# Performance work log

Hardware: AMD Instinct MI355X
Metric: run time of the kernel (lower is better)

Reference implementation:

```python
import jax, jax.numpy as jnp
import numpy as np

# Dims matching init_kwargs / input_specs
H = 64   # latent_size (GRU hidden)
L = 64   # rnn_layers
D = 128  # input_size
B = 128  # batch
T = 256  # sequence length


def setup_inputs() -> dict:
    key = jax.random.key(0)
    ks = jax.random.split(key, 13)
    s = 1.0 / np.sqrt(H)  # PyTorch GRU/Linear default init scale
    u = lambda k, shp: jax.random.uniform(k, shp, jnp.float32, -s, s)
    return {
        "context": jax.random.normal(ks[0], (B, T, D), jnp.float32),
        # encoder GRU params; layer 0 consumes D, layers 1..L-1 consume H
        "enc_Wih0": u(ks[1], (3 * H, D)),
        "enc_Wih": u(ks[2], (L - 1, 3 * H, H)),
        "enc_Whh": u(ks[3], (L, 3 * H, H)),
        "enc_bih": u(ks[4], (L, 3 * H)),
        "enc_bhh": u(ks[5], (L, 3 * H)),
        # decoder GRU params
        "dec_Wih0": u(ks[6], (3 * H, D)),
        "dec_Wih": u(ks[7], (L - 1, 3 * H, H)),
        "dec_Whh": u(ks[8], (L, 3 * H, H)),
        "dec_bih": u(ks[9], (L, 3 * H)),
        "dec_bhh": u(ks[10], (L, 3 * H)),
        # output projection
        "Wo": u(ks[11], (D, H)),
        "bo": u(ks[12], (D,)),
    }


def _gru_cell(x, h, Wih, Whh, bih, bhh):
    # PyTorch gate order: r, z, n
    gi = x @ Wih.T + bih            # (B, 3H)
    gh = h @ Whh.T + bhh            # (B, 3H)
    ir, iz, inn = jnp.split(gi, 3, axis=-1)
    hr, hz, hn = jnp.split(gh, 3, axis=-1)
    r = jax.nn.sigmoid(ir + hr)
    z = jax.nn.sigmoid(iz + hz)
    n = jnp.tanh(inn + r * hn)
    return (1.0 - z) * n + z * h


def _run_gru(X, h0, Wih0, Wih, Whh, bih, bhh):
    # X: (B, T, D); h0: (L, B, H). Returns (top-layer outputs (B,T,H), final hidden (L,B,H)).
    def layer_step(x_in, lp):
        h_prev, W_ih, W_hh, b_i, b_h = lp
        h_new = _gru_cell(x_in, h_prev, W_ih, W_hh, b_i, b_h)
        return h_new, h_new

    @jax.checkpoint
    def step(hs, x_t):
        h_first = _gru_cell(x_t, hs[0], Wih0, Whh[0], bih[0], bhh[0])
        top, hs_rest = jax.lax.scan(
            layer_step, h_first, (hs[1:], Wih, Whh[1:], bih[1:], bhh[1:]))
        return jnp.concatenate([h_first[None], hs_rest], axis=0), top

    hs_final, outs = jax.lax.scan(step, h0, jnp.swapaxes(X, 0, 1))
    return jnp.swapaxes(outs, 0, 1), hs_final


def reference(context, enc_Wih0, enc_Wih, enc_Whh, enc_bih, enc_bhh,
              dec_Wih0, dec_Wih, dec_Whh, dec_bih, dec_bhh, Wo, bo):
    Bc = context.shape[0]
    h0 = jnp.zeros((L, Bc, H), context.dtype)
    # encoder: only final hidden state is used
    _, h_n = _run_gru(context, h0, enc_Wih0, enc_Wih, enc_Whh, enc_bih, enc_bhh)
    # teacher forcing (ratio=1.0): decoder input at step i is X[:, i-1], zeros at i=0
    dec_in = jnp.concatenate([jnp.zeros_like(context[:, :1]), context[:, :-1]], axis=1)
    dec_out, _ = _run_gru(dec_in, h_n, dec_Wih0, dec_Wih, dec_Whh, dec_bih, dec_bhh)
    return dec_out @ Wo.T + bo  # (B, T, D)
```

## Files before the change

kernel.cpp:

```cpp
#include <hip/hip_runtime.h>
#include <stdint.h>

typedef uint16_t u16;
typedef unsigned long long u64;
typedef __attribute__((ext_vector_type(8))) short short8;
typedef __attribute__((ext_vector_type(4))) float f32x4;

#define SCOPE __HIP_MEMORY_SCOPE_AGENT
#define FSTRIDE 16
#define FLD(p) __hip_atomic_load((p), __ATOMIC_RELAXED, SCOPE)
#define FST(p, v) __hip_atomic_store((p), (v), __ATOMIC_RELAXED, SCOPE)

template <int N> struct IC { static constexpr int value = N; };

static __device__ __forceinline__ float bf2f(u16 b) {
  union { uint32_t u; float f; } x; x.u = ((uint32_t)b) << 16; return x.f;
}
static __device__ __forceinline__ u16 f2bf(float f) {
  union { float f; uint32_t u; } x; x.f = f;
  uint32_t u = x.u;
  u += 0x7fffu + ((u >> 16) & 1u);
  return (u16)(u >> 16);
}
static __device__ __forceinline__ float sigm(float x) {
  return __builtin_amdgcn_rcpf(1.f + __expf(-x));
}
static __device__ __forceinline__ float tanhf_(float x) {
  return 1.f - 2.f * __builtin_amdgcn_rcpf(1.f + __expf(2.f * x));
}
static __device__ __forceinline__ void lds_barrier() {
  asm volatile("s_waitcnt lgkmcnt(0)\n\ts_barrier" ::: "memory");
}
#define DRAIN0() asm volatile("s_waitcnt vmcnt(0)" ::: "memory")
static __device__ __forceinline__ int imin(int a, int b) { return a < b ? a : b; }

#define OFF_WHA 0
#define OFF_WHB 12288
#define OFF_WIB 24576
#define OFF_WIA 36864
#define OFF_WO  49152

template <int CHE, int CHD>
__global__ __launch_bounds__(256, 1) void gru_pipeline(
    const void* ctx_,
    const void* eWih0_, const void* eWih_, const void* eWhh_,
    const void* ebih_,  const void* ebhh_,
    const void* dWih0_, const void* dWih_, const void* dWhh_,
    const void* dbih_,  const void* dbhh_,
    const void* Wo_,    const void* bo_,   void* out_,
    int* __restrict__ pflag, int* __restrict__ cflag,
    u64* __restrict__ xbufW, int RW, int RE)
{
  const int tid  = threadIdx.x;
  const int lane = tid & 63;
  const int q    = tid >> 6;
  const int lo   = lane & 15;
  const int hi   = lane >> 4;
  const int blk  = blockIdx.x;
  const int P    = blk >> 3;
  const int g    = blk & 7;
  const int LA   = 2 * P;
  const int LB   = 2 * P + 1;
  const int NKCA = (P == 0) ? 4 : 2;
  u64* xbufE = (u64*)out_;

  extern __shared__ __align__(16) u16 dynlds[];

  __shared__ __align__(16) u16 hbA[2][16 * 72];
  __shared__ __align__(16) u16 hbB[2][16 * 72];
  __shared__ __align__(16) u16 xstA[2][16 * 72];
  __shared__ int s_cnt, s_fin, s_cn;
  if (tid == 0) { s_cnt = 0; s_fin = 0; s_cn = 0; }
  for (int i = tid; i < 16 * 72; i += 256) {
    hbA[0][i] = 0; hbA[1][i] = 0; hbB[0][i] = 0; hbB[1][i] = 0;
    xstA[0][i] = 0; xstA[1][i] = 0;
  }
  __syncthreads();
  {
    u16 v = ((const u16*)ebih_)[2 * tid];
    int e = (v >> 7) & 0xFF;
    if (e >= 100 && e <= 126) atomicAdd(&s_cnt, 1);
  }
  __syncthreads();
  const bool bf = (s_cnt >= 128);

  auto ld8 = [&](const void* p, int idx) -> short8 {
    if (bf) return *(const short8*)((const u16*)p + idx);
    const float* f = (const float*)p + idx;
    short8 r;
#pragma unroll
    for (int j = 0; j < 8; ++j) r[j] = (short)f2bf(f[j]);
    return r;
  };
  auto ld1 = [&](const void* p, int idx) -> float {
    return bf ? bf2f(((const u16*)p)[idx]) : ((const float*)p)[idx];
  };

  const int T0 = q, T1 = 4 + q, T2 = 8 + q;

  short8 zf8 = {0,0,0,0,0,0,0,0};
  float  bov[2] = {0.f, 0.f};
  float brzA[2], binA, bhnA;
  float brzB[2], binB, bhnB;

  auto stage_w = [&](int offU16, const void* W, int gidx0, int NT, int KC, int K) {
    for (int nt = q; nt < NT; nt += 4)
      for (int kc = 0; kc < KC; ++kc) {
        short8 v = ld8(W, gidx0 + (nt*16 + lo)*K + kc*32 + hi*8);
        *(short8*)(dynlds + offU16 + (nt*KC + kc)*512 + lane*8) = v;
      }
  };

  auto load_phase = [&](int ph) {
    const void* WH  = ph ? dWhh_ : eWhh_;
    const void* WIs = ph ? dWih_ : eWih_;
    const void* WI0 = ph ? dWih0_ : eWih0_;
    const void* bi  = ph ? dbih_ : ebih_;
    const void* bh  = ph ? dbhh_ : ebhh_;
    stage_w(OFF_WHA, WH, LA*192*64, 12, 2, 64);
    stage_w(OFF_WHB, WH, LB*192*64, 12, 2, 64);
    stage_w(OFF_WIB, WIs, LA*192*64, 12, 2, 64);
    if (LA == 0) stage_w(OFF_WIA, WI0, 0, 12, 4, 128);
    else         stage_w(OFF_WIA, WIs, (LA-1)*192*64, 12, 2, 64);
    brzA[0] = ld1(bi, LA*192 + T0*16 + lo) + ld1(bh, LA*192 + T0*16 + lo);
    brzA[1] = ld1(bi, LA*192 + T1*16 + lo) + ld1(bh, LA*192 + T1*16 + lo);
    binA    = ld1(bi, LA*192 + T2*16 + lo);
    bhnA    = ld1(bh, LA*192 + T2*16 + lo);
    brzB[0] = ld1(bi, LB*192 + T0*16 + lo) + ld1(bh, LB*192 + T0*16 + lo);
    brzB[1] = ld1(bi, LB*192 + T1*16 + lo) + ld1(bh, LB*192 + T1*16 + lo);
    binB    = ld1(bi, LB*192 + T2*16 + lo);
    bhnB    = ld1(bh, LB*192 + T2*16 + lo);
  };
  load_phase(0);
  if (P == 31) {
    stage_w(OFF_WO, Wo_, 0, 8, 2, 64);
    bov[0] = ld1(bo_, 32*q + lo);
    bov[1] = ld1(bo_, 32*q + 16 + lo);
  }

  const int oWhA0 = OFF_WHA + T0*1024 + lane*8;
  const int oWhA1 = OFF_WHA + T1*1024 + lane*8;
  const int oWhA2 = OFF_WHA + T2*1024 + lane*8;
  const int oWhB0 = OFF_WHB + T0*1024 + lane*8;
  const int oWhB1 = OFF_WHB + T1*1024 + lane*8;
  const int oWhB2 = OFF_WHB + T2*1024 + lane*8;
  const int oWiB0 = OFF_WIB + T0*1024 + lane*8;
  const int oWiB1 = OFF_WIB + T1*1024 + lane*8;
  const int oWiB2 = OFF_WIB + T2*1024 + lane*8;
  const int oWiA0 = OFF_WIA + T0*(NKCA*512) + lane*8;
  const int oWiA1 = OFF_WIA + T1*(NKCA*512) + lane*8;
  const int oWiA2 = OFF_WIA + T2*(NKCA*512) + lane*8;
  const int oWo0  = OFF_WO + (2*q + 0)*1024 + lane*8;
  const int oWo1  = OFF_WO + (2*q + 1)*1024 + lane*8;

  auto WF = [&](int off, int kc) -> short8 {
    return *(const short8*)(dynlds + off + kc*512);
  };

  auto do_proj = [&](int tprev, const u16* hs) {
    f32x4 pacc[2];
#pragma unroll
    for (int ct = 0; ct < 2; ++ct) { float v = bov[ct]; f32x4 tv = {v,v,v,v}; pacc[ct] = tv; }
#pragma unroll
    for (int kc = 0; kc < 2; ++kc) {
      short8 hA = *(const short8*)(hs + lo*72 + kc*32 + hi*8);
      pacc[0] = __builtin_amdgcn_mfma_f32_16x16x32_bf16(hA, WF(oWo0, kc), pacc[0], 0, 0, 0);
      pacc[1] = __builtin_amdgcn_mfma_f32_16x16x32_bf16(hA, WF(oWo1, kc), pacc[1], 0, 0, 0);
    }
#pragma unroll
    for (int ct = 0; ct < 2; ++ct) {
      int n = 32*q + 16*ct + lo;
#pragma unroll
      for (int p = 0; p < 4; ++p) {
        int b = 16*g + hi*4 + p;
        size_t idx = ((size_t)b * 256 + (tprev - 256)) * 128 + n;
        float v = fminf(64.f, fmaxf(-64.f, pacc[ct][p]));
        if (bf) ((u16*)out_)[idx] = f2bf(v);
        else    ((float*)out_)[idx] = v;
      }
    }
  };

  float hprevA[4], hprevB[4];
#pragma unroll
  for (int p = 0; p < 4; ++p) { hprevA[p] = 0.f; hprevB[p] = 0.f; }

  const int brow = 16*g + lo;

  const int eIn  = (P > 0 ? P - 1 : 0) * 8 + g;
  const int eOut = (P < 31 ? P : 30) * 8 + g;
  int* fin   = pflag + eIn  * FSTRIDE;
  int* fout  = pflag + eOut * FSTRIDE;
  int* cself = cflag + (P * 8 + g) * FSTRIDE;
  int* cnext = cflag + ((P < 31 ? P + 1 : 31) * 8 + g) * FSTRIDE;

  int budget = 1 << 22;
  const int srow = 4 * (tid & 3);
  const int scol = tid >> 2;

  int f0 = 0, f1 = 0, f2 = 0, f3 = 0;
  int c0 = 0, c1 = 0, c2 = 0, c3 = 0;

  __syncthreads();

  auto span = [&](auto chc, const int tbase, const int cbase, const int RC, const bool dec) {
    constexpr int CH  = decltype(chc)::value;
    constexpr int PTT = (CH >= 2) ? CH - 2 : 0;
    const int NC   = 256 / CH;
    const int RM   = dec ? (RW - 1) : (RE - 1);
    const int toff = dec ? 256 : 0;
    const u64* rbi = dec ? (xbufW + (size_t)eIn  * ((size_t)RW * 256))
                         : (xbufE + (size_t)eIn  * ((size_t)RE * 256));
    u64*       rbo = dec ? (xbufW + (size_t)eOut * ((size_t)RW * 256))
                         : (xbufE + (size_t)eOut * ((size_t)RE * 256));

#pragma unroll 1
    for (int k = 0; k < NC; ++k) {
      const int ck    = cbase + k;
      const int t0    = tbase + k * CH;
      const int fneed = ck + 1;
      const int need  = (k >= RC) ? (cbase + k + 1 - RC) : 0;

      const bool slowF = (P > 0)  && (s_fin < fneed);
      const bool slowC = (P < 31) && (need > 0) && (s_cn < need);
      if (slowF || slowC) {
        if (tid == 0) {
          if (slowF) {
            int v = 0;
            while (budget > 0) {
              int a = FLD(fin + 0), b = FLD(fin + 1), c = FLD(fin + 2), d = FLD(fin + 3);
              v = imin(imin(a, b), imin(c, d));
              if (v >= fneed) break;
              --budget; __builtin_amdgcn_s_sleep(2);
            }
            s_fin = v;
          }
          if (slowC) {
            int v = 0;
            while (budget > 0) {
              int a = FLD(cnext + 0), b = FLD(cnext + 1), c = FLD(cnext + 2), d = FLD(cnext + 3);
              v = imin(imin(a, b), imin(c, d));
              if (v >= need) break;
              --budget; __builtin_amdgcn_s_sleep(2);
            }
            s_cn = v;
          }
        }
        lds_barrier();
      }

      u64 pa[CH];
#pragma unroll
      for (int j = 0; j < CH; ++j) pa[j] = 0;
      if (P > 0) {
#pragma unroll
        for (int j = 0; j < CH; ++j)
          pa[j] = FLD(rbi + (size_t)((t0 + j - toff) & RM) * 256 + tid);
      }

#pragma unroll
      for (int tt = 0; tt < CH; ++tt) {
        const int t = t0 + tt;

        if (P > 0) {
          u16* xd = xstA[t & 1];
#pragma unroll
          for (int p = 0; p < 4; ++p)
            xd[(srow + p) * 72 + scol] = (u16)(pa[tt] >> (16 * p));
        }

        lds_barrier();

        if (tt == PTT && tid == 0) {
          if (P > 0)  { f0 = FLD(fin + 0); f1 = FLD(fin + 1); f2 = FLD(fin + 2); f3 = FLD(fin + 3); }
          if (P < 31) { c0 = FLD(cnext + 0); c1 = FLD(cnext + 1); c2 = FLD(cnext + 2); c3 = FLD(cnext + 3); }
        }

        if (P == 31 && t >= 257) do_proj(t - 1, hbB[(t + 1) & 1]);

        f32x4 ar, az, ain, ahn;
        { float v;
          v = brzA[0]; ar  = (f32x4){v,v,v,v};
          v = brzA[1]; az  = (f32x4){v,v,v,v};
          v = binA;    ain = (f32x4){v,v,v,v};
          v = bhnA;    ahn = (f32x4){v,v,v,v}; }
        const u16* hsA = hbA[(t + 1) & 1];
#pragma unroll
        for (int kc = 0; kc < 2; ++kc) {
          short8 hA = *(const short8*)(hsA + lo*72 + kc*32 + hi*8);
          ar  = __builtin_amdgcn_mfma_f32_16x16x32_bf16(hA, WF(oWhA0, kc), ar,  0, 0, 0);
          az  = __builtin_amdgcn_mfma_f32_16x16x32_bf16(hA, WF(oWhA1, kc), az,  0, 0, 0);
          ahn = __builtin_amdgcn_mfma_f32_16x16x32_bf16(hA, WF(oWhA2, kc), ahn, 0, 0, 0);
        }
        short8 xfA[4] = {zf8, zf8, zf8, zf8};
        if (P > 0) {
          const u16* xs = xstA[t & 1];
#pragma unroll
          for (int kc = 0; kc < 2; ++kc)
            xfA[kc] = *(const short8*)(xs + lo*72 + kc*32 + hi*8);
        } else {
          int tx = (t < 256) ? t : ((t == 256) ? 0 : t - 257);
#pragma unroll
          for (int kc = 0; kc < 4; ++kc)
            xfA[kc] = ld8(ctx_, (brow * 256 + tx) * 128 + kc*32 + hi*8);
        }
        if (!(P == 0 && t == 256)) {
#pragma unroll
          for (int kc = 0; kc < 4; ++kc) {
            if (kc < NKCA) {
              ar  = __builtin_amdgcn_mfma_f32_16x16x32_bf16(xfA[kc], WF(oWiA0, kc), ar,  0, 0, 0);
              az  = __builtin_amdgcn_mfma_f32_16x16x32_bf16(xfA[kc], WF(oWiA1, kc), az,  0, 0, 0);
              ain = __builtin_amdgcn_mfma_f32_16x16x32_bf16(xfA[kc], WF(oWiA2, kc), ain, 0, 0, 0);
            }
          }
        }
        u16 hAb[4];
#pragma unroll
        for (int p = 0; p < 4; ++p) {
          float r = sigm(ar[p]);
          float z = sigm(az[p]);
          float n = tanhf_(ain[p] + r * ahn[p]);
          float h = n + z * (hprevA[p] - n);
          h = fminf(1.f, fmaxf(-1.f, h));
          hprevA[p] = h;
          hAb[p] = f2bf(h);
        }

        if (tt == CH - 1 && tid == 0) {
          if (P > 0)  s_fin = imin(imin(f0, f1), imin(f2, f3));
          if (P < 31) s_cn  = imin(imin(c0, c1), imin(c2, c3));
        }

        {
          u16* hd = hbA[t & 1];
#pragma unroll
          for (int p = 0; p < 4; ++p)
            hd[(hi*4 + p) * 72 + q*16 + lo] = hAb[p];
        }

        lds_barrier();

        { float v;
          v = brzB[0]; ar  = (f32x4){v,v,v,v};
          v = brzB[1]; az  = (f32x4){v,v,v,v};
          v = binB;    ain = (f32x4){v,v,v,v};
          v = bhnB;    ahn = (f32x4){v,v,v,v}; }
        const u16* hsB = hbB[(t + 1) & 1];
        const u16* xsB = hbA[t & 1];
#pragma unroll
        for (int kc = 0; kc < 2; ++kc) {
          short8 hB = *(const short8*)(hsB + lo*72 + kc*32 + hi*8);
          short8 xB = *(const short8*)(xsB + lo*72 + kc*32 + hi*8);
          ar  = __builtin_amdgcn_mfma_f32_16x16x32_bf16(hB, WF(oWhB0, kc), ar,  0, 0, 0);
          az  = __builtin_amdgcn_mfma_f32_16x16x32_bf16(hB, WF(oWhB1, kc), az,  0, 0, 0);
          ahn = __builtin_amdgcn_mfma_f32_16x16x32_bf16(hB, WF(oWhB2, kc), ahn, 0, 0, 0);
          ar  = __builtin_amdgcn_mfma_f32_16x16x32_bf16(xB, WF(oWiB0, kc), ar,  0, 0, 0);
          az  = __builtin_amdgcn_mfma_f32_16x16x32_bf16(xB, WF(oWiB1, kc), az,  0, 0, 0);
          ain = __builtin_amdgcn_mfma_f32_16x16x32_bf16(xB, WF(oWiB2, kc), ain, 0, 0, 0);
        }
        u16 hBb[4];
#pragma unroll
        for (int p = 0; p < 4; ++p) {
          float r = sigm(ar[p]);
          float z = sigm(az[p]);
          float n = tanhf_(ain[p] + r * ahn[p]);
          float h = n + z * (hprevB[p] - n);
          h = fminf(1.f, fmaxf(-1.f, h));
          hprevB[p] = h;
          hBb[p] = f2bf(h);
        }
        {
          u16* hd = hbB[t & 1];
#pragma unroll
          for (int p = 0; p < 4; ++p)
            hd[(hi*4 + p) * 72 + q*16 + lo] = hBb[p];
        }
        if (P < 31) {
          u64 da = (u64)hBb[0] | ((u64)hBb[1] << 16) | ((u64)hBb[2] << 32) | ((u64)hBb[3] << 48);
          FST(rbo + (size_t)((t - toff) & RM) * 256 + (16*q + lo)*4 + hi, da);
        }
      }

      if (P < 31) {
        DRAIN0();
        if (lane == 0) FST(fout + q, ck + 1);
      }
      if (P > 0 && lane == 0) FST(cself + q, ck + 1);
    }
  };

  span(IC<CHE>{}, 0, 0, RE / CHE, false);
  __syncthreads();
  load_phase(1);
  __syncthreads();
  {
    int rcd = RW / CHD; if (rcd < 1) rcd = 1;
    span(IC<CHD>{}, 256, 256 / CHE, rcd, true);
  }

  lds_barrier();
  if (P == 31) do_proj(511, hbB[1]);
}

extern "C" void kernel_launch(void* const* d_in, const int* in_sizes, int n_in,
                              void* d_out, int out_size, void* d_ws, size_t ws_size,
                              hipStream_t stream)
{
  char* ws = (char*)d_ws;
  int* pflag = (int*)ws;
  int* cflag = (int*)(ws + 16384);
  u64* xbufW = (u64*)(ws + 32768);

  const size_t per_slot = (size_t)31 * 8 * 2048;
  size_t avail = (ws_size > 32768) ? ws_size - 32768 : 0;
  int RW = 1;
  for (int r = 128; r >= 1; r >>= 1)
    if ((size_t)r * per_slot <= avail) { RW = r; break; }
  int RE = 1;
  for (int r = 16; r >= 1; r >>= 1)
    if ((size_t)r * per_slot <= (size_t)out_size) { RE = r; break; }

  const int dyn = 122880;
  static int attr_done = 0;
  if (!attr_done) {
    hipFuncSetAttribute(reinterpret_cast<const void*>(gru_pipeline<4,4>),
                        hipFuncAttributeMaxDynamicSharedMemorySize, dyn);
    hipFuncSetAttribute(reinterpret_cast<const void*>(gru_pipeline<4,2>),
                        hipFuncAttributeMaxDynamicSharedMemorySize, dyn);
    hipFuncSetAttribute(reinterpret_cast<const void*>(gru_pipeline<4,1>),
                        hipFuncAttributeMaxDynamicSharedMemorySize, dyn);
    hipFuncSetAttribute(reinterpret_cast<const void*>(gru_pipeline<1,1>),
                        hipFuncAttributeMaxDynamicSharedMemorySize, dyn);
    attr_done = 1;
  }

  hipMemsetAsync(ws, 0, 32768, stream);

#define LAUNCH(CE, CD)                                                     \
  gru_pipeline<CE, CD><<<256, 256, dyn, stream>>>(                         \
      d_in[0], d_in[1], d_in[2], d_in[3], d_in[4], d_in[5],                \
      d_in[6], d_in[7], d_in[8], d_in[9], d_in[10], d_in[11], d_in[12],    \
      d_out, pflag, cflag, xbufW, RW, RE)

  if (RE >= 4) {
    if      (RW >= 8) LAUNCH(4, 4);
    else if (RW >= 4) LAUNCH(4, 2);
    else              LAUNCH(4, 1);
  } else {
    LAUNCH(1, 1);
  }
#undef LAUNCH
  (void)in_sizes; (void)n_in;
}
```

Measured before the change: 1.769 ms.

## Split layer pair into two warp groups skewed by one timestep

Doubles the block to 512 threads. The first four waves compute layer A at step t while the second four compute layer B at step t-1, so the two layers of a pair run concurrently instead of back to back. Inter-layer x loads are prefetched one step ahead, context loads for P==0 are software-pipelined, and the output projection is moved onto the B group. Chunk sizes and flag protocols change to match (encoder chunk 2, extra handshake slack). This risks more barrier overhead, higher register pressure at 512 threads, and subtle ordering bugs in the flag and ring-buffer protocol.

```diff
diff --git a/kernel.cpp b/kernel.cpp
--- a/kernel.cpp
+++ b/kernel.cpp
@@ -41,7 +41,7 @@
 #define OFF_WO  49152
 
 template <int CHE, int CHD>
-__global__ __launch_bounds__(256, 1) void gru_pipeline(
+__global__ __launch_bounds__(512, 1) void gru_pipeline(
     const void* ctx_,
     const void* eWih0_, const void* eWih_, const void* eWhh_,
     const void* ebih_,  const void* ebhh_,
@@ -52,15 +52,16 @@
     u64* __restrict__ xbufW, int RW, int RE)
 {
   const int tid  = threadIdx.x;
+  const bool isX = (tid < 256);
   const int lane = tid & 63;
-  const int q    = tid >> 6;
+  const int qg   = (tid >> 6) & 3;
+  const int w8   = tid >> 6;
   const int lo   = lane & 15;
   const int hi   = lane >> 4;
   const int blk  = blockIdx.x;
   const int P    = blk >> 3;
   const int g    = blk & 7;
   const int LA   = 2 * P;
-  const int LB   = 2 * P + 1;
   const int NKCA = (P == 0) ? 4 : 2;
   u64* xbufE = (u64*)out_;
 
@@ -71,15 +72,15 @@
   __shared__ __align__(16) u16 xstA[2][16 * 72];
   __shared__ int s_cnt, s_fin, s_cn;
   if (tid == 0) { s_cnt = 0; s_fin = 0; s_cn = 0; }
-  for (int i = tid; i < 16 * 72; i += 256) {
+  for (int i = tid; i < 16 * 72; i += 512) {
     hbA[0][i] = 0; hbA[1][i] = 0; hbB[0][i] = 0; hbB[1][i] = 0;
     xstA[0][i] = 0; xstA[1][i] = 0;
   }
   __syncthreads();
   {
-    u16 v = ((const u16*)ebih_)[2 * tid];
+    u16 v = ((const u16*)ebih_)[2 * (tid & 255)];
     int e = (v >> 7) & 0xFF;
-    if (e >= 100 && e <= 126) atomicAdd(&s_cnt, 1);
+    if (e >= 100 && e <= 126 && isX) atomicAdd(&s_cnt, 1);
   }
   __syncthreads();
   const bool bf = (s_cnt >= 128);
@@ -96,15 +97,15 @@
     return bf ? bf2f(((const u16*)p)[idx]) : ((const float*)p)[idx];
   };
 
-  const int T0 = q, T1 = 4 + q, T2 = 8 + q;
+  const int T0 = qg, T1 = 4 + qg, T2 = 8 + qg;
 
   short8 zf8 = {0,0,0,0,0,0,0,0};
   float  bov[2] = {0.f, 0.f};
-  float brzA[2], binA, bhnA;
-  float brzB[2], binB, bhnB;
+  float brzA[2] = {0,0}, binA = 0, bhnA = 0;
+  float brzB[2] = {0,0}, binB = 0, bhnB = 0;
 
   auto stage_w = [&](int offU16, const void* W, int gidx0, int NT, int KC, int K) {
-    for (int nt = q; nt < NT; nt += 4)
+    for (int nt = w8; nt < NT; nt += 8)
       for (int kc = 0; kc < KC; ++kc) {
         short8 v = ld8(W, gidx0 + (nt*16 + lo)*K + kc*32 + hi*8);
         *(short8*)(dynlds + offU16 + (nt*KC + kc)*512 + lane*8) = v;
@@ -118,24 +119,27 @@
     const void* bi  = ph ? dbih_ : ebih_;
     const void* bh  = ph ? dbhh_ : ebhh_;
     stage_w(OFF_WHA, WH, LA*192*64, 12, 2, 64);
-    stage_w(OFF_WHB, WH, LB*192*64, 12, 2, 64);
+    stage_w(OFF_WHB, WH, (LA+1)*192*64, 12, 2, 64);
     stage_w(OFF_WIB, WIs, LA*192*64, 12, 2, 64);
     if (LA == 0) stage_w(OFF_WIA, WI0, 0, 12, 4, 128);
     else         stage_w(OFF_WIA, WIs, (LA-1)*192*64, 12, 2, 64);
-    brzA[0] = ld1(bi, LA*192 + T0*16 + lo) + ld1(bh, LA*192 + T0*16 + lo);
-    brzA[1] = ld1(bi, LA*192 + T1*16 + lo) + ld1(bh, LA*192 + T1*16 + lo);
-    binA    = ld1(bi, LA*192 + T2*16 + lo);
-    bhnA    = ld1(bh, LA*192 + T2*16 + lo);
-    brzB[0] = ld1(bi, LB*192 + T0*16 + lo) + ld1(bh, LB*192 + T0*16 + lo);
-    brzB[1] = ld1(bi, LB*192 + T1*16 + lo) + ld1(bh, LB*192 + T1*16 + lo);
-    binB    = ld1(bi, LB*192 + T2*16 + lo);
-    bhnB    = ld1(bh, LB*192 + T2*16 + lo);
+    if (isX) {
+      brzA[0] = ld1(bi, LA*192 + T0*16 + lo) + ld1(bh, LA*192 + T0*16 + lo);
+      brzA[1] = ld1(bi, LA*192 + T1*16 + lo) + ld1(bh, LA*192 + T1*16 + lo);
+      binA    = ld1(bi, LA*192 + T2*16 + lo);
+      bhnA    = ld1(bh, LA*192 + T2*16 + lo);
+    } else {
+      const int LB = LA + 1;
+      brzB[0] = ld1(bi, LB*192 + T0*16 + lo) + ld1(bh, LB*192 + T0*16 + lo);
+      brzB[1] = ld1(bi, LB*192 + T1*16 + lo) + ld1(bh, LB*192 + T1*16 + lo);
+      binB    = ld1(bi, LB*192 + T2*16 + lo);
+      bhnB    = ld1(bh, LB*192 + T2*16 + lo);
+    }
   };
   load_phase(0);
   if (P == 31) {
     stage_w(OFF_WO, Wo_, 0, 8, 2, 64);
-    bov[0] = ld1(bo_, 32*q + lo);
-    bov[1] = ld1(bo_, 32*q + 16 + lo);
+    if (!isX) { bov[0] = ld1(bo_, 32*qg + lo); bov[1] = ld1(bo_, 32*qg + 16 + lo); }
   }
 
   const int oWhA0 = OFF_WHA + T0*1024 + lane*8;
@@ -150,8 +154,8 @@
   const int oWiA0 = OFF_WIA + T0*(NKCA*512) + lane*8;
   const int oWiA1 = OFF_WIA + T1*(NKCA*512) + lane*8;
   const int oWiA2 = OFF_WIA + T2*(NKCA*512) + lane*8;
-  const int oWo0  = OFF_WO + (2*q + 0)*1024 + lane*8;
-  const int oWo1  = OFF_WO + (2*q + 1)*1024 + lane*8;
+  const int oWo0  = OFF_WO + (2*qg + 0)*1024 + lane*8;
+  const int oWo1  = OFF_WO + (2*qg + 1)*1024 + lane*8;
 
   auto WF = [&](int off, int kc) -> short8 {
     return *(const short8*)(dynlds + off + kc*512);
@@ -169,7 +173,7 @@
     }
 #pragma unroll
     for (int ct = 0; ct < 2; ++ct) {
-      int n = 32*q + 16*ct + lo;
+      int n = 32*qg + 16*ct + lo;
 #pragma unroll
       for (int p = 0; p < 4; ++p) {
         int b = 16*g + hi*4 + p;
@@ -181,10 +185,7 @@
     }
   };
 
-  float hprevA[4], hprevB[4];
-#pragma unroll
-  for (int p = 0; p < 4; ++p) { hprevA[p] = 0.f; hprevB[p] = 0.f; }
-
+  float hprevA[4] = {0,0,0,0}, hprevB[4] = {0,0,0,0};
   const int brow = 16*g + lo;
 
   const int eIn  = (P > 0 ? P - 1 : 0) * 8 + g;
@@ -194,198 +195,248 @@
   int* cself = cflag + (P * 8 + g) * FSTRIDE;
   int* cnext = cflag + ((P < 31 ? P + 1 : 31) * 8 + g) * FSTRIDE;
 
+  auto raddr = [&](int t) -> const u64* {
+    return (t < 256)
+      ? (xbufE + (size_t)eIn * ((size_t)RE * 256) + (size_t)(t & (RE-1)) * 256)
+      : (xbufW + (size_t)eIn * ((size_t)RW * 256) + (size_t)((t-256) & (RW-1)) * 256);
+  };
+  auto waddr = [&](int t) -> u64* {
+    return (t < 256)
+      ? (xbufE + (size_t)eOut * ((size_t)RE * 256) + (size_t)(t & (RE-1)) * 256)
+      : (xbufW + (size_t)eOut * ((size_t)RW * 256) + (size_t)((t-256) & (RW-1)) * 256);
+  };
+
   int budget = 1 << 22;
   const int srow = 4 * (tid & 3);
   const int scol = tid >> 2;
 
-  int f0 = 0, f1 = 0, f2 = 0, f3 = 0;
-  int c0 = 0, c1 = 0, c2 = 0, c3 = 0;
+  int f0=0,f1=0,f2=0,f3=0, c0=0,c1=0,c2=0,c3=0;
+  short8 cfx[4] = {zf8, zf8, zf8, zf8};
+
+  auto doB = [&](int s) {
+    f32x4 br, bz, bin2, bhn;
+    { float v;
+      v = brzB[0]; br   = (f32x4){v,v,v,v};
+      v = brzB[1]; bz   = (f32x4){v,v,v,v};
+      v = binB;    bin2 = (f32x4){v,v,v,v};
+      v = bhnB;    bhn  = (f32x4){v,v,v,v}; }
+    const u16* hsB = hbB[(s + 1) & 1];
+    const u16* xsB = hbA[s & 1];
+#pragma unroll
+    for (int kc = 0; kc < 2; ++kc) {
+      short8 hB = *(const short8*)(hsB + lo*72 + kc*32 + hi*8);
+      short8 xB = *(const short8*)(xsB + lo*72 + kc*32 + hi*8);
+      br   = __builtin_amdgcn_mfma_f32_16x16x32_bf16(hB, WF(oWhB0, kc), br,   0, 0, 0);
+      bz   = __builtin_amdgcn_mfma_f32_16x16x32_bf16(hB, WF(oWhB1, kc), bz,   0, 0, 0);
+      bhn  = __builtin_amdgcn_mfma_f32_16x16x32_bf16(hB, WF(oWhB2, kc), bhn,  0, 0, 0);
+      br   = __builtin_amdgcn_mfma_f32_16x16x32_bf16(xB, WF(oWiB0, kc), br,   0, 0, 0);
+      bz   = __builtin_amdgcn_mfma_f32_16x16x32_bf16(xB, WF(oWiB1, kc), bz,   0, 0, 0);
+      bin2 = __builtin_amdgcn_mfma_f32_16x16x32_bf16(xB, WF(oWiB2, kc), bin2, 0, 0, 0);
+    }
+    u16 hBb[4];
+#pragma unroll
+    for (int p = 0; p < 4; ++p) {
+      float r = sigm(br[p]);
+      float z = sigm(bz[p]);
+      float n = tanhf_(bin2[p] + r * bhn[p]);
+      float h = n + z * (hprevB[p] - n);
+      h = fminf(1.f, fmaxf(-1.f, h));
+      hprevB[p] = h;
+      hBb[p] = f2bf(h);
+    }
+    u16* hd = hbB[s & 1];
+#pragma unroll
+    for (int p = 0; p < 4; ++p)
+      hd[(hi*4 + p) * 72 + qg*16 + lo] = hBb[p];
+    if (P < 31) {
+      u64 da = (u64)hBb[0] | ((u64)hBb[1] << 16) | ((u64)hBb[2] << 32) | ((u64)hBb[3] << 48);
+      FST(waddr(s) + (16*qg + lo)*4 + hi, da);
+    }
+  };
 
   __syncthreads();
 
   auto span = [&](auto chc, const int tbase, const int cbase, const int RC, const bool dec) {
     constexpr int CH  = decltype(chc)::value;
     constexpr int PTT = (CH >= 2) ? CH - 2 : 0;
-    const int NC   = 256 / CH;
-    const int RM   = dec ? (RW - 1) : (RE - 1);
-    const int toff = dec ? 256 : 0;
-    const u64* rbi = dec ? (xbufW + (size_t)eIn  * ((size_t)RW * 256))
-                         : (xbufE + (size_t)eIn  * ((size_t)RE * 256));
-    u64*       rbo = dec ? (xbufW + (size_t)eOut * ((size_t)RW * 256))
-                         : (xbufE + (size_t)eOut * ((size_t)RE * 256));
+    const int NC = 256 / CH;
+
+    if (P > 0) {
+      if (tid == 0) {
+        int v = s_fin;
+        if (v < cbase + 1) {
+          while (budget > 0) {
+            int a = FLD(fin+0), b = FLD(fin+1), c = FLD(fin+2), d = FLD(fin+3);
+            v = imin(imin(a, b), imin(c, d));
+            if (v >= cbase + 1) break;
+            --budget; __builtin_amdgcn_s_sleep(2);
+          }
+          s_fin = v;
+        }
+      }
+      __syncthreads();
+      if (isX) {
+        u64 r0 = FLD(raddr(tbase) + tid);
+        u16* xd = xstA[tbase & 1];
+#pragma unroll
+        for (int p = 0; p < 4; ++p) xd[(srow + p) * 72 + scol] = (u16)(r0 >> (16 * p));
+      }
+    }
+    if (P == 0 && isX) {
+      int tx = (tbase < 256) ? tbase : 0;
+#pragma unroll
+      for (int kc = 0; kc < 4; ++kc) cfx[kc] = ld8(ctx_, (brow*256 + tx)*128 + kc*32 + hi*8);
+    }
 
 #pragma unroll 1
     for (int k = 0; k < NC; ++k) {
-      const int ck    = cbase + k;
-      const int t0    = tbase + k * CH;
-      const int fneed = ck + 1;
-      const int need  = (k >= RC) ? (cbase + k + 1 - RC) : 0;
-
-      const bool slowF = (P > 0)  && (s_fin < fneed);
-      const bool slowC = (P < 31) && (need > 0) && (s_cn < need);
-      if (slowF || slowC) {
-        if (tid == 0) {
-          if (slowF) {
-            int v = 0;
-            while (budget > 0) {
-              int a = FLD(fin + 0), b = FLD(fin + 1), c = FLD(fin + 2), d = FLD(fin + 3);
-              v = imin(imin(a, b), imin(c, d));
-              if (v >= fneed) break;
-              --budget; __builtin_amdgcn_s_sleep(2);
-            }
-            s_fin = v;
-          }
-          if (slowC) {
-            int v = 0;
-            while (budget > 0) {
-              int a = FLD(cnext + 0), b = FLD(cnext + 1), c = FLD(cnext + 2), d = FLD(cnext + 3);
-              v = imin(imin(a, b), imin(c, d));
-              if (v >= need) break;
-              --budget; __builtin_amdgcn_s_sleep(2);
-            }
-            s_cn = v;
-          }
-        }
-        lds_barrier();
-      }
-
-      u64 pa[CH];
-#pragma unroll
-      for (int j = 0; j < CH; ++j) pa[j] = 0;
-      if (P > 0) {
-#pragma unroll
-        for (int j = 0; j < CH; ++j)
-          pa[j] = FLD(rbi + (size_t)((t0 + j - toff) & RM) * 256 + tid);
-      }
+      const int t0 = tbase + k * CH;
+      const int ck = cbase + k;
+      const int fneed = ck + 2 - ((dec && k == NC - 1) ? 1 : 0);
+      const int need  = (k >= RC) ? (ck + 1 - RC) : 0;
+      u64 ra[CH];
+#pragma unroll
+      for (int j = 0; j < CH; ++j) ra[j] = 0;
 
 #pragma unroll
       for (int tt = 0; tt < CH; ++tt) {
         const int t = t0 + tt;
-
-        if (P > 0) {
-          u16* xd = xstA[t & 1];
-#pragma unroll
-          for (int p = 0; p < 4; ++p)
-            xd[(srow + p) * 72 + scol] = (u16)(pa[tt] >> (16 * p));
+        lds_barrier();
+
+        if (tt == 0) {
+          int vf = s_fin, vc = s_cn;
+          const bool slowF = (P > 0)  && (vf < fneed);
+          const bool slowC = (P < 31) && (need > 0) && (vc < need);
+          if (slowF || slowC) {
+            if (tid == 0) {
+              if (slowF) {
+                int v = 0;
+                while (budget > 0) {
+                  int a = FLD(fin+0), b = FLD(fin+1), c = FLD(fin+2), d = FLD(fin+3);
+                  v = imin(imin(a, b), imin(c, d));
+                  if (v >= fneed) break;
+                  --budget; __builtin_amdgcn_s_sleep(2);
+                }
+                s_fin = v;
+              }
+              if (slowC) {
+                int v = 0;
+                while (budget > 0) {
+                  int a = FLD(cnext+0), b = FLD(cnext+1), c = FLD(cnext+2), d = FLD(cnext+3);
+                  v = imin(imin(a, b), imin(c, d));
+                  if (v >= need) break;
+                  --budget; __builtin_amdgcn_s_sleep(2);
+                }
+                s_cn = v;
+              }
+            }
+            lds_barrier();
+          }
+          if (isX && P > 0) {
+#pragma unroll
+            for (int j = 0; j < CH; ++j)
+              if (t0 + 1 + j <= 511) ra[j] = FLD(raddr(t0 + 1 + j) + tid);
+          }
         }
 
-        lds_barrier();
-
-        if (tt == PTT && tid == 0) {
-          if (P > 0)  { f0 = FLD(fin + 0); f1 = FLD(fin + 1); f2 = FLD(fin + 2); f3 = FLD(fin + 3); }
-          if (P < 31) { c0 = FLD(cnext + 0); c1 = FLD(cnext + 1); c2 = FLD(cnext + 2); c3 = FLD(cnext + 3); }
-        }
-
-        if (P == 31 && t >= 257) do_proj(t - 1, hbB[(t + 1) & 1]);
-
-        f32x4 ar, az, ain, ahn;
-        { float v;
-          v = brzA[0]; ar  = (f32x4){v,v,v,v};
-          v = brzA[1]; az  = (f32x4){v,v,v,v};
-          v = binA;    ain = (f32x4){v,v,v,v};
-          v = bhnA;    ahn = (f32x4){v,v,v,v}; }
-        const u16* hsA = hbA[(t + 1) & 1];
-#pragma unroll
-        for (int kc = 0; kc < 2; ++kc) {
-          short8 hA = *(const short8*)(hsA + lo*72 + kc*32 + hi*8);
-          ar  = __builtin_amdgcn_mfma_f32_16x16x32_bf16(hA, WF(oWhA0, kc), ar,  0, 0, 0);
-          az  = __builtin_amdgcn_mfma_f32_16x16x32_bf16(hA, WF(oWhA1, kc), az,  0, 0, 0);
-          ahn = __builtin_amdgcn_mfma_f32_16x16x32_bf16(hA, WF(oWhA2, kc), ahn, 0, 0, 0);
-        }
-        short8 xfA[4] = {zf8, zf8, zf8, zf8};
-        if (P > 0) {
-          const u16* xs = xstA[t & 1];
-#pragma unroll
-          for (int kc = 0; kc < 2; ++kc)
-            xfA[kc] = *(const short8*)(xs + lo*72 + kc*32 + hi*8);
+        if (isX) {
+          if (tt == CH - 1 && tid == 0) {
+            if (P > 0)  s_fin = imin(imin(f0, f1), imin(f2, f3));
+            if (P < 31) s_cn  = imin(imin(c0, c1), imin(c2, c3));
+          }
+          if (tt == PTT && tid == 0) {
+            if (P > 0)  { f0 = FLD(fin+0); f1 = FLD(fin+1); f2 = FLD(fin+2); f3 = FLD(fin+3); }
+            if (P < 31) { c0 = FLD(cnext+0); c1 = FLD(cnext+1); c2 = FLD(cnext+2); c3 = FLD(cnext+3); }
+          }
+
+          f32x4 ar, az, ain, ahn;
+          { float v;
+            v = brzA[0]; ar  = (f32x4){v,v,v,v};
+            v = brzA[1]; az  = (f32x4){v,v,v,v};
+            v = binA;    ain = (f32x4){v,v,v,v};
+            v = bhnA;    ahn = (f32x4){v,v,v,v}; }
+          const u16* hsA = hbA[(t + 1) & 1];
+#pragma unroll
+          for (int kc = 0; kc < 2; ++kc) {
+            short8 hA = *(const short8*)(hsA + lo*72 + kc*32 + hi*8);
+            ar  = __builtin_amdgcn_mfma_f32_16x16x32_bf16(hA, WF(oWhA0, kc), ar,  0, 0, 0);
+            az  = __builtin_amdgcn_mfma_f32_16x16x32_bf16(hA, WF(oWhA1, kc), az,  0, 0, 0);
+            ahn = __builtin_amdgcn_mfma_f32_16x16x32_bf16(hA, WF(oWhA2, kc), ahn, 0, 0, 0);
+          }
+          short8 xfA[4] = {zf8, zf8, zf8, zf8};
+          if (P > 0) {
+            const u16* xs = xstA[t & 1];
+#pragma unroll
+            for (int kc = 0; kc < 2; ++kc)
+              xfA[kc] = *(const short8*)(xs + lo*72 + kc*32 + hi*8);
+          } else {
+#pragma unroll
+            for (int kc = 0; kc < 4; ++kc) xfA[kc] = cfx[kc];
+          }
+          if (!(P == 0 && t == 256)) {
+#pragma unroll
+            for (int kc = 0; kc < 4; ++kc) {
+              if (kc < NKCA) {
+                ar  = __builtin_amdgcn_mfma_f32_16x16x32_bf16(xfA[kc], WF(oWiA0, kc), ar,  0, 0, 0);
+                az  = __builtin_amdgcn_mfma_f32_16x16x32_bf16(xfA[kc], WF(oWiA1, kc), az,  0, 0, 0);
+                ain = __builtin_amdgcn_mfma_f32_16x16x32_bf16(xfA[kc], WF(oWiA2, kc), ain, 0, 0, 0);
+              }
+            }
+          }
+          u16 hAb[4];
+#pragma unroll
+          for (int p = 0; p < 4; ++p) {
+            float r = sigm(ar[p]);
+            float z = sigm(az[p]);
+            float n = tanhf_(ain[p] + r * ahn[p]);
+            float h = n + z * (hprevA[p] - n);
+            h = fminf(1.f, fmaxf(-1.f, h));
+            hprevA[p] = h;
+            hAb[p] = f2bf(h);
+          }
+          {
+            u16* hd = hbA[t & 1];
+#pragma unroll
+            for (int p = 0; p < 4; ++p)
+              hd[(hi*4 + p) * 72 + qg*16 + lo] = hAb[p];
+          }
+          if (P == 0) {
+            int tn = t + 1;
+            if (tn <= 511) {
+              int tx = (tn < 256) ? tn : ((tn == 256) ? 0 : tn - 257);
+#pragma unroll
+              for (int kc = 0; kc < 4; ++kc)
+                cfx[kc] = ld8(ctx_, (brow*256 + tx)*128 + kc*32 + hi*8);
+            }
+          }
+          if (P > 0 && t < 511) {
+            u64 r = ra[tt];
+            u16* xd = xstA[(t + 1) & 1];
+#pragma unroll
+            for (int p = 0; p < 4; ++p) xd[(srow + p) * 72 + scol] = (u16)(r >> (16 * p));
+          }
+          if (tt == CH - 1 && P > 0) {
+            DRAIN0();
+            if (lane == 0) FST(cself + qg, ck + 1);
+          }
         } else {
-          int tx = (t < 256) ? t : ((t == 256) ? 0 : t - 257);
-#pragma unroll
-          for (int kc = 0; kc < 4; ++kc)
-            xfA[kc] = ld8(ctx_, (brow * 256 + tx) * 128 + kc*32 + hi*8);
-        }
-        if (!(P == 0 && t == 256)) {
-#pragma unroll
-          for (int kc = 0; kc < 4; ++kc) {
-            if (kc < NKCA) {
-              ar  = __builtin_amdgcn_mfma_f32_16x16x32_bf16(xfA[kc], WF(oWiA0, kc), ar,  0, 0, 0);
-              az  = __builtin_amdgcn_mfma_f32_16x16x32_bf16(xfA[kc], WF(oWiA1, kc), az,  0, 0, 0);
-              ain = __builtin_amdgcn_mfma_f32_16x16x32_bf16(xfA[kc], WF(oWiA2, kc), ain, 0, 0, 0);
-            }
-          }
-        }
-        u16 hAb[4];
-#pragma unroll
-        for (int p = 0; p < 4; ++p) {
-          float r = sigm(ar[p]);
-          float z = sigm(az[p]);
-          float n = tanhf_(ain[p] + r * ahn[p]);
-          float h = n + z * (hprevA[p] - n);
-          h = fminf(1.f, fmaxf(-1.f, h));
-          hprevA[p] = h;
-          hAb[p] = f2bf(h);
-        }
-
-        if (tt == CH - 1 && tid == 0) {
-          if (P > 0)  s_fin = imin(imin(f0, f1), imin(f2, f3));
-          if (P < 31) s_cn  = imin(imin(c0, c1), imin(c2, c3));
-        }
-
-        {
-          u16* hd = hbA[t & 1];
-#pragma unroll
-          for (int p = 0; p < 4; ++p)
-            hd[(hi*4 + p) * 72 + q*16 + lo] = hAb[p];
-        }
-
-        lds_barrier();
-
-        { float v;
-          v = brzB[0]; ar  = (f32x4){v,v,v,v};
-          v = brzB[1]; az  = (f32x4){v,v,v,v};
-          v = binB;    ain = (f32x4){v,v,v,v};
-          v = bhnB;    ahn = (f32x4){v,v,v,v}; }
-        const u16* hsB = hbB[(t + 1) & 1];
-        const u16* xsB = hbA[t & 1];
-#pragma unroll
-        for (int kc = 0; kc < 2; ++kc) {
-          short8 hB = *(const short8*)(hsB + lo*72 + kc*32 + hi*8);
-          short8 xB = *(const short8*)(xsB + lo*72 + kc*32 + hi*8);
-          ar  = __builtin_amdgcn_mfma_f32_16x16x32_bf16(hB, WF(oWhB0, kc), ar,  0, 0, 0);
-          az  = __builtin_amdgcn_mfma_f32_16x16x32_bf16(hB, WF(oWhB1, kc), az,  0, 0, 0);
-          ahn = __builtin_amdgcn_mfma_f32_16x16x32_bf16(hB, WF(oWhB2, kc), ahn, 0, 0, 0);
-          ar  = __builtin_amdgcn_mfma_f32_16x16x32_bf16(xB, WF(oWiB0, kc), ar,  0, 0, 0);
-          az  = __builtin_amdgcn_mfma_f32_16x16x32_bf16(xB, WF(oWiB1, kc), az,  0, 0, 0);
-          ain = __builtin_amdgcn_mfma_f32_16x16x32_bf16(xB, WF(oWiB2, kc), ain, 0, 0, 0);
-        }
-        u16 hBb[4];
-#pragma unroll
-        for (int p = 0; p < 4; ++p) {
-          float r = sigm(ar[p]);
-          float z = sigm(az[p]);
-          float n = tanhf_(ain[p] + r * ahn[p]);
-          float h = n + z * (hprevB[p] - n);
-          h = fminf(1.f, fmaxf(-1.f, h));
-          hprevB[p] = h;
-          hBb[p] = f2bf(h);
-        }
-        {
-          u16* hd = hbB[t & 1];
-#pragma unroll
-          for (int p = 0; p < 4; ++p)
-            hd[(hi*4 + p) * 72 + q*16 + lo] = hBb[p];
-        }
-        if (P < 31) {
-          u64 da = (u64)hBb[0] | ((u64)hBb[1] << 16) | ((u64)hBb[2] << 32) | ((u64)hBb[3] << 48);
-          FST(rbo + (size_t)((t - toff) & RM) * 256 + (16*q + lo)*4 + hi, da);
+          if (P == 31 && dec && t >= 258) do_proj(t - 2, hbB[t & 1]);
+          if (t - 1 >= tbase) doB(t - 1);
+          if (P < 31 && tt == 0 && k > 0) {
+            DRAIN0();
+            if (lane == 0) FST(fout + qg, ck);
+          }
         }
       }
-
+    }
+
+    lds_barrier();
+    if (!isX) {
+      doB(tbase + 255);
       if (P < 31) {
         DRAIN0();
-        if (lane == 0) FST(fout + q, ck + 1);
+        if (lane == 0) FST(fout + qg, cbase + NC);
       }
-      if (P > 0 && lane == 0) FST(cself + q, ck + 1);
     }
   };
 
@@ -399,7 +450,10 @@
   }
 
   lds_barrier();
-  if (P == 31) do_proj(511, hbB[1]);
+  if (P == 31 && !isX) {
+    do_proj(510, hbB[0]);
+    do_proj(511, hbB[1]);
+  }
 }
 
 extern "C" void kernel_launch(void* const* d_in, const int* in_sizes, int n_in,
@@ -423,13 +477,11 @@
   const int dyn = 122880;
   static int attr_done = 0;
   if (!attr_done) {
-    hipFuncSetAttribute(reinterpret_cast<const void*>(gru_pipeline<4,4>),
+    hipFuncSetAttribute(reinterpret_cast<const void*>(gru_pipeline<2,4>),
                         hipFuncAttributeMaxDynamicSharedMemorySize, dyn);
-    hipFuncSetAttribute(reinterpret_cast<const void*>(gru_pipeline<4,2>),
+    hipFuncSetAttribute(reinterpret_cast<const void*>(gru_pipeline<2,2>),
                         hipFuncAttributeMaxDynamicSharedMemorySize, dyn);
-    hipFuncSetAttribute(reinterpret_cast<const void*>(gru_pipeline<4,1>),
-                        hipFuncAttributeMaxDynamicSharedMemorySize, dyn);
-    hipFuncSetAttribute(reinterpret_cast<const void*>(gru_pipeline<1,1>),
+    hipFuncSetAttribute(reinterpret_cast<const void*>(gru_pipeline<2,1>),
                         hipFuncAttributeMaxDynamicSharedMemorySize, dyn);
     attr_done = 1;
   }
@@ -437,18 +489,14 @@
   hipMemsetAsync(ws, 0, 32768, stream);
 
 #define LAUNCH(CE, CD)                                                     \
-  gru_pipeline<CE, CD><<<256, 256, dyn, stream>>>(                         \
+  gru_pipeline<CE, CD><<<256, 512, dyn, stream>>>(                         \
       d_in[0], d_in[1], d_in[2], d_in[3], d_in[4], d_in[5],                \
       d_in[6], d_in[7], d_in[8], d_in[9], d_in[10], d_in[11], d_in[12],    \
       d_out, pflag, cflag, xbufW, RW, RE)
 
-  if (RE >= 4) {
-    if      (RW >= 8) LAUNCH(4, 4);
-    else if (RW >= 4) LAUNCH(4, 2);
-    else              LAUNCH(4, 1);
-  } else {
-    LAUNCH(1, 1);
-  }
+  if      (RW >= 16) LAUNCH(2, 4);
+  else if (RW >= 8)  LAUNCH(2, 2);
+  else               LAUNCH(2, 1);
 #undef LAUNCH
   (void)in_sizes; (void)n_in;
 }
```

Measured after the change: 1.708 ms. -3.4%, faster.
